# Kernel tuning notes

Hardware: AMD Instinct MI355X
Metric: run time of the kernel (lower is better)

Reference implementation:

```python
import jax, jax.numpy as jnp
import numpy as np

N_NODES = 50000
N_EDGES = 600000
F_IN, HID, N_CLS = 128, 128, 40
NEG_SLOPE = 0.2


def _gat_conv(x, src, dst, W, a_src, a_dst, b, num_nodes):
    # x: [N, Fin] -> h: [N, H]  (heads=1 PyG GATConv)
    h = x @ W
    s_src = h @ a_src  # [N]
    s_dst = h @ a_dst  # [N]
    e = jax.nn.leaky_relu(s_src[src] + s_dst[dst], NEG_SLOPE)  # [E]
    # numerically-stable softmax over incoming edges per destination node
    m = jax.ops.segment_max(e, dst, num_segments=num_nodes)  # [N]
    ex = jnp.exp(e - m[dst])
    denom = jax.ops.segment_sum(ex, dst, num_segments=num_nodes)  # [N]
    alpha = ex / denom[dst]  # [E]
    out = jax.ops.segment_sum(alpha[:, None] * h[src], dst, num_segments=num_nodes)
    return out + b


def setup_inputs() -> dict:
    key = jax.random.key(0)
    ks = jax.random.split(key, 10)
    x = jax.random.normal(ks[0], (N_NODES, F_IN), dtype=jnp.float32)
    edge_index = jax.random.randint(ks[1], (2, N_EDGES), 0, N_NODES, dtype=jnp.int64)
    sd = lambda fin: 1.0 / np.sqrt(fin)
    return {
        "x": x,
        "edge_index": edge_index,
        "W1": jax.random.normal(ks[2], (F_IN, HID), dtype=jnp.float32) * sd(F_IN),
        "a1_src": jax.random.normal(ks[3], (HID,), dtype=jnp.float32) * sd(HID),
        "a1_dst": jax.random.normal(ks[4], (HID,), dtype=jnp.float32) * sd(HID),
        "b1": jnp.zeros((HID,), dtype=jnp.float32),
        "W2": jax.random.normal(ks[5], (HID, HID), dtype=jnp.float32) * sd(HID),
        "a2_src": jax.random.normal(ks[6], (HID,), dtype=jnp.float32) * sd(HID),
        "a2_dst": jax.random.normal(ks[7], (HID,), dtype=jnp.float32) * sd(HID),
        "b2": jnp.zeros((HID,), dtype=jnp.float32),
        "Wl": jax.random.normal(ks[8], (HID, N_CLS), dtype=jnp.float32) * sd(HID),
        "bl": jnp.zeros((N_CLS,), dtype=jnp.float32),
    }


def reference(x, edge_index, W1, a1_src, a1_dst, b1, W2, a2_src, a2_dst, b2, Wl, bl):
    n = x.shape[0]
    # PyG GATConv adds self loops by default
    loops = jnp.arange(n, dtype=edge_index.dtype)
    src = jnp.concatenate([edge_index[0], loops])
    dst = jnp.concatenate([edge_index[1], loops])
    h = jax.nn.relu(_gat_conv(x, src, dst, W1, a1_src, a1_dst, b1, n))
    # F.dropout(training=self.training): eval mode -> identity
    h = _gat_conv(h, src, dst, W2, a2_src, a2_dst, b2, n)
    logits = jax.nn.log_softmax(h @ Wl + bl, axis=1)
    return (logits, edge_index)
```

## Files before the change

kernel.cpp:

```cpp
#include <hip/hip_runtime.h>
#include <hip/hip_bf16.h>
#include <math.h>

#define N_NODES 50000
#define N_EDGES 600000
#define TOT_E   (N_EDGES + N_NODES)
#define FDIM    128
#define HROW    64
#define NCLS    40
#define SCAN_B  1024

typedef __attribute__((ext_vector_type(4))) float  f32x4;
typedef __attribute__((ext_vector_type(8))) __bf16 bf16x8;
union FragU { uint32_t u[4]; bf16x8 v; };

__device__ inline float bf16_lo(uint32_t u) { return __uint_as_float(u << 16); }
__device__ inline float bf16_hi(uint32_t u) { return __uint_as_float(u & 0xffff0000u); }
__device__ inline uint32_t bf16_pack(float a, float b) {
    uint32_t ua = __float_as_uint(a), ub = __float_as_uint(b);
    uint32_t ra = (ua + 0x7fffu + ((ua >> 16) & 1u)) >> 16;
    uint32_t rb = (ub + 0x7fffu + ((ub >> 16) & 1u)) >> 16;
    return ra | (rb << 16);
}

__global__ void init_counts(int* __restrict__ counts) {
    int i = blockIdx.x * blockDim.x + threadIdx.x;
    if (i < N_NODES) counts[i] = 1;
}

__global__ void hist_kernel(const int* __restrict__ ei, int* __restrict__ counts) {
    int i = blockIdx.x * blockDim.x + threadIdx.x;
    if (i >= N_EDGES / 4) return;
    int4 d = ((const int4*)(ei + N_EDGES))[i];
    atomicAdd(&counts[d.x], 1);
    atomicAdd(&counts[d.y], 1);
    atomicAdd(&counts[d.z], 1);
    atomicAdd(&counts[d.w], 1);
}

__global__ void scan1_kernel(const int* __restrict__ counts, int* __restrict__ excl,
                             int* __restrict__ bsums, int n) {
    __shared__ int ws[16];
    int gid = blockIdx.x * SCAN_B + threadIdx.x;
    int wv = threadIdx.x >> 6, lane = threadIdx.x & 63;
    int v = (gid < n) ? counts[gid] : 0;
    int incl = v;
    #pragma unroll
    for (int off = 1; off < 64; off <<= 1) {
        int t = __shfl_up(incl, off, 64);
        if (lane >= off) incl += t;
    }
    if (lane == 63) ws[wv] = incl;
    __syncthreads();
    int woff = 0;
    for (int i = 0; i < wv; i++) woff += ws[i];
    if (gid < n) excl[gid] = woff + incl - v;
    if (threadIdx.x == SCAN_B - 1) bsums[blockIdx.x] = woff + incl;
}

__global__ void scan3_kernel(int* __restrict__ rowptr, const int* __restrict__ bsums,
                             int* __restrict__ cursor, int n, int total) {
    __shared__ int base_s;
    if (threadIdx.x < 64) {
        int v = (threadIdx.x < (int)blockIdx.x) ? bsums[threadIdx.x] : 0;
        #pragma unroll
        for (int off = 32; off > 0; off >>= 1) v += __shfl_down(v, off, 64);
        if (threadIdx.x == 0) base_s = v;
    }
    __syncthreads();
    int base = base_s;
    int gid = blockIdx.x * SCAN_B + threadIdx.x;
    if (gid < n) {
        int v = rowptr[gid] + base;
        rowptr[gid] = v;
        cursor[gid] = v;
    }
    if (gid == 0) rowptr[n] = total;
}

#define SCAT_T ((N_EDGES / 4) + N_NODES)
__global__ void scatter_kernel(const int* __restrict__ ei, int* __restrict__ cursor,
                               int* __restrict__ adj) {
    int i = blockIdx.x * blockDim.x + threadIdx.x;
    if (i >= SCAT_T) return;
    if (i < N_EDGES / 4) {
        int4 s4 = ((const int4*)ei)[i];
        int4 d4 = ((const int4*)(ei + N_EDGES))[i];
        adj[atomicAdd(&cursor[d4.x], 1)] = s4.x;
        adj[atomicAdd(&cursor[d4.y], 1)] = s4.y;
        adj[atomicAdd(&cursor[d4.z], 1)] = s4.z;
        adj[atomicAdd(&cursor[d4.w], 1)] = s4.w;
    } else {
        int nd = i - N_EDGES / 4;
        adj[atomicAdd(&cursor[nd], 1)] = nd;
    }
}

__global__ void prep_wa(const float* __restrict__ W1, const float* __restrict__ a1s,
                        const float* __restrict__ a1d, const float* __restrict__ W2,
                        const float* __restrict__ a2s, const float* __restrict__ a2d,
                        float* __restrict__ wa) {
    int t = threadIdx.x;
    int vec = t >> 7, k = t & 127;
    const float* W = (vec < 2) ? W1 : W2;
    const float* a = (vec == 0) ? a1s : (vec == 1) ? a1d : (vec == 2) ? a2s : a2d;
    float s = 0.f;
    #pragma unroll 4
    for (int j = 0; j < FDIM; j += 4) {
        float4 wv = *(const float4*)&W[k * FDIM + j];
        float4 av = *(const float4*)&a[j];
        s += wv.x * av.x + wv.y * av.y + wv.z * av.z + wv.w * av.w;
    }
    wa[vec * FDIM + k] = s;
}

__global__ void pack_x(const float* __restrict__ x, uint32_t* __restrict__ Xp) {
    int i = blockIdx.x * blockDim.x + threadIdx.x;
    if (i >= N_NODES * HROW) return;
    float2 v = ((const float2*)x)[i];
    Xp[i] = bf16_pack(v.x, v.y);
}

__global__ void prep_wfrag(const float* __restrict__ W1, const float* __restrict__ W2,
                           uint32_t* __restrict__ wf1, uint32_t* __restrict__ wf2) {
    int t = blockIdx.x * blockDim.x + threadIdx.x;
    if (t >= 4096) return;
    const float* W = (t < 2048) ? W1 : W2;
    uint32_t*   wf = (t < 2048) ? wf1 : wf2;
    int q = t & 2047;
    int lane = q & 63, nt = (q >> 6) & 7, kt = q >> 9;
    int n = nt * 16 + (lane & 15), g = lane >> 4;
    uint32_t frag[4];
    #pragma unroll
    for (int d = 0; d < 4; d++) {
        int kb = kt * 32 + 4 * g + (d & 1) * 2 + (d >> 1) * 16;
        frag[d] = bf16_pack(W[kb * FDIM + n], W[(kb + 1) * FDIM + n]);
    }
    ((uint4*)wf)[(kt * 8 + nt) * 64 + lane] = *(uint4*)frag;
}

__global__ __launch_bounds__(256) void mfma_gemm(
        const uint32_t* __restrict__ Xp, const uint32_t* __restrict__ wf,
        uint32_t* __restrict__ H) {
    int lane = threadIdx.x & 63, wv = threadIdx.x >> 6;
    int row0 = blockIdx.x * 64 + wv * 16;
    if (row0 >= N_NODES) return;
    int r = lane & 15, g = lane >> 4;

    const uint32_t* xrow = Xp + (size_t)(row0 + r) * HROW + 2 * g;
    FragU af[4];
    #pragma unroll
    for (int kt = 0; kt < 4; kt++) {
        uint2 lo = *(const uint2*)(xrow + kt * 16);
        uint2 hi = *(const uint2*)(xrow + kt * 16 + 8);
        af[kt].u[0] = lo.x; af[kt].u[1] = lo.y;
        af[kt].u[2] = hi.x; af[kt].u[3] = hi.y;
    }

    f32x4 acc[8] = {};
    #pragma unroll
    for (int kt = 0; kt < 4; kt++) {
        #pragma unroll
        for (int nt = 0; nt < 8; nt++) {
            FragU bfr;
            *(uint4*)bfr.u = ((const uint4*)wf)[(kt * 8 + nt) * 64 + lane];
            acc[nt] = __builtin_amdgcn_mfma_f32_16x16x32_bf16(af[kt].v, bfr.v, acc[nt], 0, 0, 0);
        }
    }

    #pragma unroll
    for (int nt = 0; nt < 8; nt++) {
        #pragma unroll
        for (int j = 0; j < 4; j++) {
            float v0 = acc[nt][j];
            float v1 = __shfl_xor(v0, 1, 64);
            if (!(r & 1)) {
                uint32_t p = bf16_pack(v0, v1);
                H[(size_t)(row0 + 4 * g + j) * HROW + nt * 8 + (r >> 1)] = p;
            }
        }
    }
}

template <bool BF16IN>
__global__ __launch_bounds__(256) void score_kernel(
        const void* __restrict__ Xin, const float* __restrict__ wa_s,
        const float* __restrict__ wa_d, float* __restrict__ ssrc,
        float* __restrict__ sdst) {
    int wv = threadIdx.x >> 6, lane = threadIdx.x & 63;
    int n = blockIdx.x * 4 + wv;
    float lo, hi;
    if (BF16IN) {
        uint32_t u = ((const uint32_t*)Xin)[(size_t)n * HROW + lane];
        lo = bf16_lo(u); hi = bf16_hi(u);
    } else {
        float2 xv = ((const float2*)Xin)[(size_t)n * (FDIM / 2) + lane];
        lo = xv.x; hi = xv.y;
    }
    float2 as = *(const float2*)&wa_s[2 * lane];
    float2 ad = *(const float2*)&wa_d[2 * lane];
    float s1 = lo * as.x + hi * as.y;
    float s2 = lo * ad.x + hi * ad.y;
    #pragma unroll
    for (int off = 32; off > 0; off >>= 1) {
        s1 += __shfl_xor(s1, off, 64);
        s2 += __shfl_xor(s2, off, 64);
    }
    if (lane == 0) { ssrc[n] = s1; sdst[n] = s2; }
}

__global__ __launch_bounds__(128) void gat_aggregate(
        const uint32_t* __restrict__ h, const float* __restrict__ ssrc,
        const float* __restrict__ sdst, const int* __restrict__ rowptr,
        const int* __restrict__ adj, const float* __restrict__ bias,
        uint32_t* __restrict__ out, int do_relu) {
    int wv = threadIdx.x >> 6, lane = threadIdx.x & 63;
    int n = blockIdx.x * 2 + wv;
    __shared__ __align__(16) float wbuf[2][64];
    __shared__ __align__(16) int   sbuf[2][64];

    int beg = rowptr[n], deg = rowptr[n + 1] - beg;
    float sd = sdst[n];

    float ax0 = 0.f, ay0 = 0.f, ax1 = 0.f, ay1 = 0.f;
    float dsum = 0.f;

    for (int base = 0; base < deg; base += 64) {
        int c = min(64, deg - base);
        if (lane < c) {
            int s = adj[beg + base + lane];
            float e = ssrc[s] + sd;
            e = (e >= 0.f) ? e : 0.2f * e;
            float w = __expf(e);
            wbuf[wv][lane] = w;
            sbuf[wv][lane] = s;
            dsum += w;
        }
        asm volatile("s_waitcnt lgkmcnt(0)" ::: "memory");

        int j = 0;
        for (; j + 8 <= c; j += 8) {
            float4 wa4 = *(const float4*)&wbuf[wv][j];
            float4 wb4 = *(const float4*)&wbuf[wv][j + 4];
            int4   sa4 = *(const int4*)&sbuf[wv][j];
            int4   sb4 = *(const int4*)&sbuf[wv][j + 4];
            uint32_t u0 = h[(size_t)sa4.x * HROW + lane];
            uint32_t u1 = h[(size_t)sa4.y * HROW + lane];
            uint32_t u2 = h[(size_t)sa4.z * HROW + lane];
            uint32_t u3 = h[(size_t)sa4.w * HROW + lane];
            uint32_t u4 = h[(size_t)sb4.x * HROW + lane];
            uint32_t u5 = h[(size_t)sb4.y * HROW + lane];
            uint32_t u6 = h[(size_t)sb4.z * HROW + lane];
            uint32_t u7 = h[(size_t)sb4.w * HROW + lane];
            ax0 += wa4.x * bf16_lo(u0); ay0 += wa4.x * bf16_hi(u0);
            ax1 += wa4.y * bf16_lo(u1); ay1 += wa4.y * bf16_hi(u1);
            ax0 += wa4.z * bf16_lo(u2); ay0 += wa4.z * bf16_hi(u2);
            ax1 += wa4.w * bf16_lo(u3); ay1 += wa4.w * bf16_hi(u3);
            ax0 += wb4.x * bf16_lo(u4); ay0 += wb4.x * bf16_hi(u4);
            ax1 += wb4.y * bf16_lo(u5); ay1 += wb4.y * bf16_hi(u5);
            ax0 += wb4.z * bf16_lo(u6); ay0 += wb4.z * bf16_hi(u6);
            ax1 += wb4.w * bf16_lo(u7); ay1 += wb4.w * bf16_hi(u7);
        }
        for (; j + 4 <= c; j += 4) {
            float4 w4 = *(const float4*)&wbuf[wv][j];
            int4   s4 = *(const int4*)&sbuf[wv][j];
            uint32_t u0 = h[(size_t)s4.x * HROW + lane];
            uint32_t u1 = h[(size_t)s4.y * HROW + lane];
            uint32_t u2 = h[(size_t)s4.z * HROW + lane];
            uint32_t u3 = h[(size_t)s4.w * HROW + lane];
            ax0 += w4.x * bf16_lo(u0); ay0 += w4.x * bf16_hi(u0);
            ax1 += w4.y * bf16_lo(u1); ay1 += w4.y * bf16_hi(u1);
            ax0 += w4.z * bf16_lo(u2); ay0 += w4.z * bf16_hi(u2);
            ax1 += w4.w * bf16_lo(u3); ay1 += w4.w * bf16_hi(u3);
        }
        for (; j < c; j++) {
            float w = wbuf[wv][j];
            int   s = sbuf[wv][j];
            uint32_t u = h[(size_t)s * HROW + lane];
            ax0 += w * bf16_lo(u); ay0 += w * bf16_hi(u);
        }
        asm volatile("" ::: "memory");
    }

    #pragma unroll
    for (int off = 32; off > 0; off >>= 1) dsum += __shfl_xor(dsum, off, 64);
    float inv = 1.f / dsum;
    float2 b2 = ((const float2*)bias)[lane];
    float vx = (ax0 + ax1) * inv + b2.x;
    float vy = (ay0 + ay1) * inv + b2.y;
    if (do_relu) { vx = fmaxf(vx, 0.f); vy = fmaxf(vy, 0.f); }
    out[(size_t)n * HROW + lane] = bf16_pack(vx, vy);
}

__global__ __launch_bounds__(128) void classifier_kernel(
        const uint32_t* __restrict__ H, const float* __restrict__ Wl,
        const float* __restrict__ bl, float* __restrict__ out) {
    __shared__ float xs[16][FDIM];
    int tid  = threadIdx.x;
    int row0 = blockIdx.x * 16;
    const uint32_t* Hp = H + (size_t)row0 * HROW;
    #pragma unroll
    for (int i = 0; i < 8; i++) {
        int idx = tid + 128 * i;
        uint32_t u = Hp[idx];
        int r = idx >> 6, cc = idx & 63;
        xs[r][2 * cc]     = bf16_lo(u);
        xs[r][2 * cc + 1] = bf16_hi(u);
    }
    __syncthreads();

    int c = tid & 63, hw = tid >> 6;
    float acc[8];
    float blc = (c < NCLS) ? bl[c] : 0.f;
    #pragma unroll
    for (int r = 0; r < 8; r++) acc[r] = blc;

    #pragma unroll 2
    for (int k = 0; k < FDIM; k += 4) {
        float w0 = 0.f, w1 = 0.f, w2 = 0.f, w3 = 0.f;
        if (c < NCLS) {
            w0 = Wl[(k + 0) * NCLS + c]; w1 = Wl[(k + 1) * NCLS + c];
            w2 = Wl[(k + 2) * NCLS + c]; w3 = Wl[(k + 3) * NCLS + c];
        }
        #pragma unroll
        for (int r = 0; r < 8; r++) {
            float4 xv = *(const float4*)&xs[hw * 8 + r][k];
            acc[r] += xv.x * w0 + xv.y * w1 + xv.z * w2 + xv.w * w3;
        }
    }
    #pragma unroll
    for (int r = 0; r < 8; r++) {
        float v = (c < NCLS) ? acc[r] : -INFINITY;
        float mx = v;
        #pragma unroll
        for (int off = 32; off > 0; off >>= 1) mx = fmaxf(mx, __shfl_xor(mx, off, 64));
        float ex = (c < NCLS) ? expf(v - mx) : 0.f;
        #pragma unroll
        for (int off = 32; off > 0; off >>= 1) ex += __shfl_xor(ex, off, 64);
        float ls = logf(ex);
        if (c < NCLS) out[(size_t)(row0 + hw * 8 + r) * NCLS + c] = v - mx - ls;
    }
}

__global__ void edge_copy_kernel(const int* __restrict__ ei, float* __restrict__ out) {
    int i = blockIdx.x * blockDim.x + threadIdx.x;
    if (i >= (2 * N_EDGES) / 4) return;
    int4 v = ((const int4*)ei)[i];
    ((float4*)out)[i] = make_float4((float)v.x, (float)v.y, (float)v.z, (float)v.w);
}

extern "C" void kernel_launch(void* const* d_in, const int* in_sizes, int n_in,
                              void* d_out, int out_size, void* d_ws, size_t ws_size,
                              hipStream_t stream) {
    const float* x   = (const float*)d_in[0];
    const int*   ei  = (const int*)d_in[1];
    const float* W1  = (const float*)d_in[2];
    const float* a1s = (const float*)d_in[3];
    const float* a1d = (const float*)d_in[4];
    const float* b1  = (const float*)d_in[5];
    const float* W2  = (const float*)d_in[6];
    const float* a2s = (const float*)d_in[7];
    const float* a2d = (const float*)d_in[8];
    const float* b2  = (const float*)d_in[9];
    const float* Wl  = (const float*)d_in[10];
    const float* bl  = (const float*)d_in[11];
    float* out = (float*)d_out;

    char* ws = (char*)d_ws;
    size_t off = 0;
    auto alloc = [&](size_t bytes) {
        void* p = ws + off;
        off = (off + bytes + 255) & ~(size_t)255;
        return p;
    };
    int*      row_ptr = (int*)alloc((N_NODES + 1) * sizeof(int));
    int*      cursor  = (int*)alloc(N_NODES * sizeof(int));
    int*      counts  = (int*)alloc(N_NODES * sizeof(int));
    int*      bsums   = (int*)alloc(64 * sizeof(int));
    int*      adj     = (int*)alloc(TOT_E * sizeof(int));
    uint32_t* Xp      = (uint32_t*)alloc((size_t)N_NODES * HROW * sizeof(uint32_t));
    uint32_t* hA      = (uint32_t*)alloc((size_t)N_NODES * HROW * sizeof(uint32_t));
    uint32_t* hB      = (uint32_t*)alloc((size_t)N_NODES * HROW * sizeof(uint32_t));
    float*    ssrc    = (float*)alloc(N_NODES * sizeof(float));
    float*    sdst    = (float*)alloc(N_NODES * sizeof(float));
    float*    wa      = (float*)alloc(4 * FDIM * sizeof(float));
    uint32_t* wf1     = (uint32_t*)alloc(2048 * 4 * sizeof(uint32_t));
    uint32_t* wf2     = (uint32_t*)alloc(2048 * 4 * sizeof(uint32_t));
    uint32_t* hC      = Xp;

    hipLaunchKernelGGL(prep_wa, dim3(1), dim3(512), 0, stream, W1, a1s, a1d, W2, a2s, a2d, wa);
    hipLaunchKernelGGL(pack_x, dim3((N_NODES * HROW) / 256), dim3(256), 0, stream, x, Xp);
    hipLaunchKernelGGL(prep_wfrag, dim3(16), dim3(256), 0, stream, W1, W2, wf1, wf2);

    hipLaunchKernelGGL(init_counts, dim3((N_NODES + 255) / 256), dim3(256), 0, stream, counts);
    hipLaunchKernelGGL(hist_kernel, dim3((N_EDGES / 4 + 255) / 256), dim3(256), 0, stream, ei, counts);
    int nscan = (N_NODES + SCAN_B - 1) / SCAN_B;
    hipLaunchKernelGGL(scan1_kernel, dim3(nscan), dim3(SCAN_B), 0, stream, counts, row_ptr, bsums, N_NODES);
    hipLaunchKernelGGL(scan3_kernel, dim3(nscan), dim3(SCAN_B), 0, stream, row_ptr, bsums, cursor, N_NODES, TOT_E);
    hipLaunchKernelGGL(scatter_kernel, dim3((SCAT_T + 255) / 256), dim3(256), 0, stream, ei, cursor, adj);

    hipLaunchKernelGGL((score_kernel<false>), dim3(N_NODES / 4), dim3(256), 0, stream,
                       (const void*)x, wa + 0, wa + FDIM, ssrc, sdst);
    hipLaunchKernelGGL(mfma_gemm, dim3((N_NODES + 63) / 64), dim3(256), 0, stream, Xp, wf1, hA);
    hipLaunchKernelGGL(gat_aggregate, dim3(N_NODES / 2), dim3(128), 0, stream,
                       hA, ssrc, sdst, row_ptr, adj, b1, hB, 1);

    hipLaunchKernelGGL((score_kernel<true>), dim3(N_NODES / 4), dim3(256), 0, stream,
                       (const void*)hB, wa + 2 * FDIM, wa + 3 * FDIM, ssrc, sdst);
    hipLaunchKernelGGL(mfma_gemm, dim3((N_NODES + 63) / 64), dim3(256), 0, stream, hB, wf2, hA);
    hipLaunchKernelGGL(gat_aggregate, dim3(N_NODES / 2), dim3(128), 0, stream,
                       hA, ssrc, sdst, row_ptr, adj, b2, hC, 0);

    hipLaunchKernelGGL(classifier_kernel, dim3(N_NODES / 16), dim3(128), 0, stream, hC, Wl, bl, out);
    hipLaunchKernelGGL(edge_copy_kernel, dim3(((2 * N_EDGES) / 4 + 255) / 256), dim3(256), 0, stream,
                       ei, out + (size_t)N_NODES * NCLS);
}
```

Measured before the change: 311.6 us.

## Fuse score computation into GEMM, merge setup/classifier kernels, widen aggregate loads

Attention scores are now computed inside the MFMA GEMM epilogue from the accumulators (dotting h with a_src/a_dst), so the separate score kernels and the W·a precompute go away. The pack_x and weight-fragment kernels are merged into one setup kernel, and init_counts becomes a memset with the self-loop +1 folded into the scan. The classifier and edge copy share one launch. The aggregation kernel now processes 4 edges per wavefront with 16-byte loads per lane and a cross-subgroup shuffle reduction. Together these cut launches and extra passes over h, at the cost of scores computed from bf16-input GEMM accumulators rather than fp32 x.

```diff
diff --git a/kernel.cpp b/kernel.cpp
--- a/kernel.cpp
+++ b/kernel.cpp
@@ -23,9 +23,32 @@
     return ra | (rb << 16);
 }
 
-__global__ void init_counts(int* __restrict__ counts) {
-    int i = blockIdx.x * blockDim.x + threadIdx.x;
-    if (i < N_NODES) counts[i] = 1;
+#define PACK_BLOCKS 12500
+__global__ __launch_bounds__(256) void setup_kernel(
+        const float* __restrict__ x, uint32_t* __restrict__ Xp,
+        const float* __restrict__ W1, const float* __restrict__ W2,
+        uint32_t* __restrict__ wf1, uint32_t* __restrict__ wf2) {
+    int b = blockIdx.x;
+    if (b < PACK_BLOCKS) {
+        int i = b * 256 + threadIdx.x;
+        float2 v = ((const float2*)x)[i];
+        Xp[i] = bf16_pack(v.x, v.y);
+        return;
+    }
+    int t = (b - PACK_BLOCKS) * 256 + threadIdx.x;
+    if (t >= 4096) return;
+    const float* W = (t < 2048) ? W1 : W2;
+    uint32_t*   wf = (t < 2048) ? wf1 : wf2;
+    int q = t & 2047;
+    int lane = q & 63, nt = (q >> 6) & 7, kt = q >> 9;
+    int n = nt * 16 + (lane & 15), g = lane >> 4;
+    uint32_t frag[4];
+    #pragma unroll
+    for (int d = 0; d < 4; d++) {
+        int kb = kt * 32 + 4 * g + (d & 1) * 2 + (d >> 1) * 16;
+        frag[d] = bf16_pack(W[kb * FDIM + n], W[(kb + 1) * FDIM + n]);
+    }
+    ((uint4*)wf)[(kt * 8 + nt) * 64 + lane] = *(uint4*)frag;
 }
 
 __global__ void hist_kernel(const int* __restrict__ ei, int* __restrict__ counts) {
@@ -43,7 +66,7 @@
     __shared__ int ws[16];
     int gid = blockIdx.x * SCAN_B + threadIdx.x;
     int wv = threadIdx.x >> 6, lane = threadIdx.x & 63;
-    int v = (gid < n) ? counts[gid] : 0;
+    int v = (gid < n) ? (counts[gid] + 1) : 0;
     int incl = v;
     #pragma unroll
     for (int off = 1; off < 64; off <<= 1) {
@@ -96,52 +119,10 @@
     }
 }
 
-__global__ void prep_wa(const float* __restrict__ W1, const float* __restrict__ a1s,
-                        const float* __restrict__ a1d, const float* __restrict__ W2,
-                        const float* __restrict__ a2s, const float* __restrict__ a2d,
-                        float* __restrict__ wa) {
-    int t = threadIdx.x;
-    int vec = t >> 7, k = t & 127;
-    const float* W = (vec < 2) ? W1 : W2;
-    const float* a = (vec == 0) ? a1s : (vec == 1) ? a1d : (vec == 2) ? a2s : a2d;
-    float s = 0.f;
-    #pragma unroll 4
-    for (int j = 0; j < FDIM; j += 4) {
-        float4 wv = *(const float4*)&W[k * FDIM + j];
-        float4 av = *(const float4*)&a[j];
-        s += wv.x * av.x + wv.y * av.y + wv.z * av.z + wv.w * av.w;
-    }
-    wa[vec * FDIM + k] = s;
-}
-
-__global__ void pack_x(const float* __restrict__ x, uint32_t* __restrict__ Xp) {
-    int i = blockIdx.x * blockDim.x + threadIdx.x;
-    if (i >= N_NODES * HROW) return;
-    float2 v = ((const float2*)x)[i];
-    Xp[i] = bf16_pack(v.x, v.y);
-}
-
-__global__ void prep_wfrag(const float* __restrict__ W1, const float* __restrict__ W2,
-                           uint32_t* __restrict__ wf1, uint32_t* __restrict__ wf2) {
-    int t = blockIdx.x * blockDim.x + threadIdx.x;
-    if (t >= 4096) return;
-    const float* W = (t < 2048) ? W1 : W2;
-    uint32_t*   wf = (t < 2048) ? wf1 : wf2;
-    int q = t & 2047;
-    int lane = q & 63, nt = (q >> 6) & 7, kt = q >> 9;
-    int n = nt * 16 + (lane & 15), g = lane >> 4;
-    uint32_t frag[4];
-    #pragma unroll
-    for (int d = 0; d < 4; d++) {
-        int kb = kt * 32 + 4 * g + (d & 1) * 2 + (d >> 1) * 16;
-        frag[d] = bf16_pack(W[kb * FDIM + n], W[(kb + 1) * FDIM + n]);
-    }
-    ((uint4*)wf)[(kt * 8 + nt) * 64 + lane] = *(uint4*)frag;
-}
-
 __global__ __launch_bounds__(256) void mfma_gemm(
         const uint32_t* __restrict__ Xp, const uint32_t* __restrict__ wf,
-        uint32_t* __restrict__ H) {
+        const float* __restrict__ a_s, const float* __restrict__ a_d,
+        uint32_t* __restrict__ H, float* __restrict__ ssrc, float* __restrict__ sdst) {
     int lane = threadIdx.x & 63, wv = threadIdx.x >> 6;
     int row0 = blockIdx.x * 64 + wv * 16;
     if (row0 >= N_NODES) return;
@@ -166,6 +147,22 @@
             *(uint4*)bfr.u = ((const uint4*)wf)[(kt * 8 + nt) * 64 + lane];
             acc[nt] = __builtin_amdgcn_mfma_f32_16x16x32_bf16(af[kt].v, bfr.v, acc[nt], 0, 0, 0);
         }
+    }
+
+    float av_s[8], av_d[8];
+    #pragma unroll
+    for (int nt = 0; nt < 8; nt++) { av_s[nt] = a_s[16 * nt + r]; av_d[nt] = a_d[16 * nt + r]; }
+    #pragma unroll
+    for (int j = 0; j < 4; j++) {
+        float ps = 0.f, pd = 0.f;
+        #pragma unroll
+        for (int nt = 0; nt < 8; nt++) { ps += acc[nt][j] * av_s[nt]; pd += acc[nt][j] * av_d[nt]; }
+        #pragma unroll
+        for (int off = 1; off < 16; off <<= 1) {
+            ps += __shfl_xor(ps, off, 64);
+            pd += __shfl_xor(pd, off, 64);
+        }
+        if (r == 0) { ssrc[row0 + 4 * g + j] = ps; sdst[row0 + 4 * g + j] = pd; }
     }
 
     #pragma unroll
@@ -182,47 +179,22 @@
     }
 }
 
-template <bool BF16IN>
-__global__ __launch_bounds__(256) void score_kernel(
-        const void* __restrict__ Xin, const float* __restrict__ wa_s,
-        const float* __restrict__ wa_d, float* __restrict__ ssrc,
-        float* __restrict__ sdst) {
-    int wv = threadIdx.x >> 6, lane = threadIdx.x & 63;
-    int n = blockIdx.x * 4 + wv;
-    float lo, hi;
-    if (BF16IN) {
-        uint32_t u = ((const uint32_t*)Xin)[(size_t)n * HROW + lane];
-        lo = bf16_lo(u); hi = bf16_hi(u);
-    } else {
-        float2 xv = ((const float2*)Xin)[(size_t)n * (FDIM / 2) + lane];
-        lo = xv.x; hi = xv.y;
-    }
-    float2 as = *(const float2*)&wa_s[2 * lane];
-    float2 ad = *(const float2*)&wa_d[2 * lane];
-    float s1 = lo * as.x + hi * as.y;
-    float s2 = lo * ad.x + hi * ad.y;
-    #pragma unroll
-    for (int off = 32; off > 0; off >>= 1) {
-        s1 += __shfl_xor(s1, off, 64);
-        s2 += __shfl_xor(s2, off, 64);
-    }
-    if (lane == 0) { ssrc[n] = s1; sdst[n] = s2; }
-}
-
 __global__ __launch_bounds__(128) void gat_aggregate(
         const uint32_t* __restrict__ h, const float* __restrict__ ssrc,
         const float* __restrict__ sdst, const int* __restrict__ rowptr,
         const int* __restrict__ adj, const float* __restrict__ bias,
         uint32_t* __restrict__ out, int do_relu) {
     int wv = threadIdx.x >> 6, lane = threadIdx.x & 63;
+    int sub = lane >> 4, l16 = lane & 15;
     int n = blockIdx.x * 2 + wv;
     __shared__ __align__(16) float wbuf[2][64];
     __shared__ __align__(16) int   sbuf[2][64];
 
     int beg = rowptr[n], deg = rowptr[n + 1] - beg;
     float sd = sdst[n];
-
-    float ax0 = 0.f, ay0 = 0.f, ax1 = 0.f, ay1 = 0.f;
+    const uint4* h4 = (const uint4*)h;
+
+    float acc[8] = {};
     float dsum = 0.f;
 
     for (int base = 0; base < deg; base += 64) {
@@ -239,62 +211,79 @@
         asm volatile("s_waitcnt lgkmcnt(0)" ::: "memory");
 
         int j = 0;
-        for (; j + 8 <= c; j += 8) {
-            float4 wa4 = *(const float4*)&wbuf[wv][j];
-            float4 wb4 = *(const float4*)&wbuf[wv][j + 4];
-            int4   sa4 = *(const int4*)&sbuf[wv][j];
-            int4   sb4 = *(const int4*)&sbuf[wv][j + 4];
-            uint32_t u0 = h[(size_t)sa4.x * HROW + lane];
-            uint32_t u1 = h[(size_t)sa4.y * HROW + lane];
-            uint32_t u2 = h[(size_t)sa4.z * HROW + lane];
-            uint32_t u3 = h[(size_t)sa4.w * HROW + lane];
-            uint32_t u4 = h[(size_t)sb4.x * HROW + lane];
-            uint32_t u5 = h[(size_t)sb4.y * HROW + lane];
-            uint32_t u6 = h[(size_t)sb4.z * HROW + lane];
-            uint32_t u7 = h[(size_t)sb4.w * HROW + lane];
-            ax0 += wa4.x * bf16_lo(u0); ay0 += wa4.x * bf16_hi(u0);
-            ax1 += wa4.y * bf16_lo(u1); ay1 += wa4.y * bf16_hi(u1);
-            ax0 += wa4.z * bf16_lo(u2); ay0 += wa4.z * bf16_hi(u2);
-            ax1 += wa4.w * bf16_lo(u3); ay1 += wa4.w * bf16_hi(u3);
-            ax0 += wb4.x * bf16_lo(u4); ay0 += wb4.x * bf16_hi(u4);
-            ax1 += wb4.y * bf16_lo(u5); ay1 += wb4.y * bf16_hi(u5);
-            ax0 += wb4.z * bf16_lo(u6); ay0 += wb4.z * bf16_hi(u6);
-            ax1 += wb4.w * bf16_lo(u7); ay1 += wb4.w * bf16_hi(u7);
-        }
-        for (; j + 4 <= c; j += 4) {
-            float4 w4 = *(const float4*)&wbuf[wv][j];
-            int4   s4 = *(const int4*)&sbuf[wv][j];
-            uint32_t u0 = h[(size_t)s4.x * HROW + lane];
-            uint32_t u1 = h[(size_t)s4.y * HROW + lane];
-            uint32_t u2 = h[(size_t)s4.z * HROW + lane];
-            uint32_t u3 = h[(size_t)s4.w * HROW + lane];
-            ax0 += w4.x * bf16_lo(u0); ay0 += w4.x * bf16_hi(u0);
-            ax1 += w4.y * bf16_lo(u1); ay1 += w4.y * bf16_hi(u1);
-            ax0 += w4.z * bf16_lo(u2); ay0 += w4.z * bf16_hi(u2);
-            ax1 += w4.w * bf16_lo(u3); ay1 += w4.w * bf16_hi(u3);
-        }
-        for (; j < c; j++) {
-            float w = wbuf[wv][j];
-            int   s = sbuf[wv][j];
-            uint32_t u = h[(size_t)s * HROW + lane];
-            ax0 += w * bf16_lo(u); ay0 += w * bf16_hi(u);
+        for (; j + 16 <= c; j += 16) {
+            float4 w4 = *(const float4*)&wbuf[wv][j + 4 * sub];
+            int4   s4 = *(const int4*)&sbuf[wv][j + 4 * sub];
+            uint4 u0 = h4[(size_t)s4.x * 16 + l16];
+            uint4 u1 = h4[(size_t)s4.y * 16 + l16];
+            uint4 u2 = h4[(size_t)s4.z * 16 + l16];
+            uint4 u3 = h4[(size_t)s4.w * 16 + l16];
+            acc[0] += w4.x * bf16_lo(u0.x) + w4.y * bf16_lo(u1.x) + w4.z * bf16_lo(u2.x) + w4.w * bf16_lo(u3.x);
+            acc[1] += w4.x * bf16_hi(u0.x) + w4.y * bf16_hi(u1.x) + w4.z * bf16_hi(u2.x) + w4.w * bf16_hi(u3.x);
+            acc[2] += w4.x * bf16_lo(u0.y) + w4.y * bf16_lo(u1.y) + w4.z * bf16_lo(u2.y) + w4.w * bf16_lo(u3.y);
+            acc[3] += w4.x * bf16_hi(u0.y) + w4.y * bf16_hi(u1.y) + w4.z * bf16_hi(u2.y) + w4.w * bf16_hi(u3.y);
+            acc[4] += w4.x * bf16_lo(u0.z) + w4.y * bf16_lo(u1.z) + w4.z * bf16_lo(u2.z) + w4.w * bf16_lo(u3.z);
+            acc[5] += w4.x * bf16_hi(u0.z) + w4.y * bf16_hi(u1.z) + w4.z * bf16_hi(u2.z) + w4.w * bf16_hi(u3.z);
+            acc[6] += w4.x * bf16_lo(u0.w) + w4.y * bf16_lo(u1.w) + w4.z * bf16_lo(u2.w) + w4.w * bf16_lo(u3.w);
+            acc[7] += w4.x * bf16_hi(u0.w) + w4.y * bf16_hi(u1.w) + w4.z * bf16_hi(u2.w) + w4.w * bf16_hi(u3.w);
+        }
+        for (; j < c; j += 4) {
+            int e = j + sub;
+            if (e < c) {
+                float w = wbuf[wv][e];
+                int   s = sbuf[wv][e];
+                uint4 u = h4[(size_t)s * 16 + l16];
+                acc[0] += w * bf16_lo(u.x); acc[1] += w * bf16_hi(u.x);
+                acc[2] += w * bf16_lo(u.y); acc[3] += w * bf16_hi(u.y);
+                acc[4] += w * bf16_lo(u.z); acc[5] += w * bf16_hi(u.z);
+                acc[6] += w * bf16_lo(u.w); acc[7] += w * bf16_hi(u.w);
+            }
         }
         asm volatile("" ::: "memory");
     }
 
     #pragma unroll
+    for (int k = 0; k < 8; k++) {
+        acc[k] += __shfl_xor(acc[k], 16, 64);
+        acc[k] += __shfl_xor(acc[k], 32, 64);
+    }
+    #pragma unroll
     for (int off = 32; off > 0; off >>= 1) dsum += __shfl_xor(dsum, off, 64);
-    float inv = 1.f / dsum;
-    float2 b2 = ((const float2*)bias)[lane];
-    float vx = (ax0 + ax1) * inv + b2.x;
-    float vy = (ay0 + ay1) * inv + b2.y;
-    if (do_relu) { vx = fmaxf(vx, 0.f); vy = fmaxf(vy, 0.f); }
-    out[(size_t)n * HROW + lane] = bf16_pack(vx, vy);
-}
-
-__global__ __launch_bounds__(128) void classifier_kernel(
+
+    if (sub == 0) {
+        float inv = 1.f / dsum;
+        float4 b0 = *(const float4*)&bias[l16 * 8];
+        float4 b1 = *(const float4*)&bias[l16 * 8 + 4];
+        float v0 = acc[0] * inv + b0.x, v1 = acc[1] * inv + b0.y;
+        float v2 = acc[2] * inv + b0.z, v3 = acc[3] * inv + b0.w;
+        float v4 = acc[4] * inv + b1.x, v5 = acc[5] * inv + b1.y;
+        float v6 = acc[6] * inv + b1.z, v7 = acc[7] * inv + b1.w;
+        if (do_relu) {
+            v0 = fmaxf(v0, 0.f); v1 = fmaxf(v1, 0.f); v2 = fmaxf(v2, 0.f); v3 = fmaxf(v3, 0.f);
+            v4 = fmaxf(v4, 0.f); v5 = fmaxf(v5, 0.f); v6 = fmaxf(v6, 0.f); v7 = fmaxf(v7, 0.f);
+        }
+        uint4 o;
+        o.x = bf16_pack(v0, v1); o.y = bf16_pack(v2, v3);
+        o.z = bf16_pack(v4, v5); o.w = bf16_pack(v6, v7);
+        ((uint4*)out)[(size_t)n * 16 + l16] = o;
+    }
+}
+
+#define CLS_BLOCKS  (N_NODES / 16)
+#define EDGE_ITEMS  ((2 * N_EDGES) / 4)
+#define EDGE_BLOCKS ((EDGE_ITEMS + 127) / 128)
+__global__ __launch_bounds__(128) void classifier_edge_kernel(
         const uint32_t* __restrict__ H, const float* __restrict__ Wl,
-        const float* __restrict__ bl, float* __restrict__ out) {
+        const float* __restrict__ bl, const int* __restrict__ ei,
+        float* __restrict__ out, float* __restrict__ eout) {
+    if (blockIdx.x >= CLS_BLOCKS) {
+        int i = (blockIdx.x - CLS_BLOCKS) * 128 + threadIdx.x;
+        if (i < EDGE_ITEMS) {
+            int4 v = ((const int4*)ei)[i];
+            ((float4*)eout)[i] = make_float4((float)v.x, (float)v.y, (float)v.z, (float)v.w);
+        }
+        return;
+    }
     __shared__ float xs[16][FDIM];
     int tid  = threadIdx.x;
     int row0 = blockIdx.x * 16;
@@ -340,13 +329,6 @@
         float ls = logf(ex);
         if (c < NCLS) out[(size_t)(row0 + hw * 8 + r) * NCLS + c] = v - mx - ls;
     }
-}
-
-__global__ void edge_copy_kernel(const int* __restrict__ ei, float* __restrict__ out) {
-    int i = blockIdx.x * blockDim.x + threadIdx.x;
-    if (i >= (2 * N_EDGES) / 4) return;
-    int4 v = ((const int4*)ei)[i];
-    ((float4*)out)[i] = make_float4((float)v.x, (float)v.y, (float)v.z, (float)v.w);
 }
 
 extern "C" void kernel_launch(void* const* d_in, const int* in_sizes, int n_in,
@@ -383,35 +365,30 @@
     uint32_t* hB      = (uint32_t*)alloc((size_t)N_NODES * HROW * sizeof(uint32_t));
     float*    ssrc    = (float*)alloc(N_NODES * sizeof(float));
     float*    sdst    = (float*)alloc(N_NODES * sizeof(float));
-    float*    wa      = (float*)alloc(4 * FDIM * sizeof(float));
     uint32_t* wf1     = (uint32_t*)alloc(2048 * 4 * sizeof(uint32_t));
     uint32_t* wf2     = (uint32_t*)alloc(2048 * 4 * sizeof(uint32_t));
     uint32_t* hC      = Xp;
 
-    hipLaunchKernelGGL(prep_wa, dim3(1), dim3(512), 0, stream, W1, a1s, a1d, W2, a2s, a2d, wa);
-    hipLaunchKernelGGL(pack_x, dim3((N_NODES * HROW) / 256), dim3(256), 0, stream, x, Xp);
-    hipLaunchKernelGGL(prep_wfrag, dim3(16), dim3(256), 0, stream, W1, W2, wf1, wf2);
-
-    hipLaunchKernelGGL(init_counts, dim3((N_NODES + 255) / 256), dim3(256), 0, stream, counts);
+    hipMemsetAsync(counts, 0, N_NODES * sizeof(int), stream);
+    hipLaunchKernelGGL(setup_kernel, dim3(PACK_BLOCKS + 16), dim3(256), 0, stream,
+                       x, Xp, W1, W2, wf1, wf2);
+
     hipLaunchKernelGGL(hist_kernel, dim3((N_EDGES / 4 + 255) / 256), dim3(256), 0, stream, ei, counts);
     int nscan = (N_NODES + SCAN_B - 1) / SCAN_B;
     hipLaunchKernelGGL(scan1_kernel, dim3(nscan), dim3(SCAN_B), 0, stream, counts, row_ptr, bsums, N_NODES);
     hipLaunchKernelGGL(scan3_kernel, dim3(nscan), dim3(SCAN_B), 0, stream, row_ptr, bsums, cursor, N_NODES, TOT_E);
     hipLaunchKernelGGL(scatter_kernel, dim3((SCAT_T + 255) / 256), dim3(256), 0, stream, ei, cursor, adj);
 
-    hipLaunchKernelGGL((score_kernel<false>), dim3(N_NODES / 4), dim3(256), 0, stream,
-                       (const void*)x, wa + 0, wa + FDIM, ssrc, sdst);
-    hipLaunchKernelGGL(mfma_gemm, dim3((N_NODES + 63) / 64), dim3(256), 0, stream, Xp, wf1, hA);
+    hipLaunchKernelGGL(mfma_gemm, dim3((N_NODES + 63) / 64), dim3(256), 0, stream,
+                       Xp, wf1, a1s, a1d, hA, ssrc, sdst);
     hipLaunchKernelGGL(gat_aggregate, dim3(N_NODES / 2), dim3(128), 0, stream,
                        hA, ssrc, sdst, row_ptr, adj, b1, hB, 1);
 
-    hipLaunchKernelGGL((score_kernel<true>), dim3(N_NODES / 4), dim3(256), 0, stream,
-                       (const void*)hB, wa + 2 * FDIM, wa + 3 * FDIM, ssrc, sdst);
-    hipLaunchKernelGGL(mfma_gemm, dim3((N_NODES + 63) / 64), dim3(256), 0, stream, hB, wf2, hA);
+    hipLaunchKernelGGL(mfma_gemm, dim3((N_NODES + 63) / 64), dim3(256), 0, stream,
+                       hB, wf2, a2s, a2d, hA, ssrc, sdst);
     hipLaunchKernelGGL(gat_aggregate, dim3(N_NODES / 2), dim3(128), 0, stream,
                        hA, ssrc, sdst, row_ptr, adj, b2, hC, 0);
 
-    hipLaunchKernelGGL(classifier_kernel, dim3(N_NODES / 16), dim3(128), 0, stream, hC, Wl, bl, out);
-    hipLaunchKernelGGL(edge_copy_kernel, dim3(((2 * N_EDGES) / 4 + 255) / 256), dim3(256), 0, stream,
-                       ei, out + (size_t)N_NODES * NCLS);
-}
+    hipLaunchKernelGGL(classifier_edge_kernel, dim3(CLS_BLOCKS + EDGE_BLOCKS), dim3(128), 0, stream,
+                       hC, Wl, bl, ei, out, out + (size_t)N_NODES * NCLS);
+}
```

After: 291.8 us. 1.07x faster.
